# Kernel tuning notes

Hardware: AMD Instinct MI355X
Metric: run time of the kernel (lower is better)

Reference implementation:

```python
import jax, jax.numpy as jnp
import numpy as np

EPS = 1e-5
N_CONV = 3
B = 2048  # number of crystals


def _bn_eval(x, gamma, beta):
    # Eval-mode BatchNorm with running_mean=0, running_var=1.
    return x * (gamma / jnp.sqrt(1.0 + EPS)) + beta


def _conv_layer(atom_fea, nbr_fea, nbr_fea_idx, W, b, g1, b1, g2, b2):
    # Canonical CGCNN ConvLayer.
    N, M = nbr_fea_idx.shape
    F = atom_fea.shape[1]
    nbr_atom = atom_fea[nbr_fea_idx]                                  # [N,M,F]
    self_atom = jnp.broadcast_to(atom_fea[:, None, :], (N, M, F))     # [N,M,F]
    total = jnp.concatenate([self_atom, nbr_atom, nbr_fea], axis=2)   # [N,M,2F+nbr]
    gated = total @ W + b                                             # [N,M,2F]
    gated = _bn_eval(gated, g1, b1)
    flt, core = jnp.split(gated, 2, axis=2)
    nbr_sumed = jnp.sum(jax.nn.sigmoid(flt) * jax.nn.softplus(core), axis=1)  # [N,F]
    nbr_sumed = _bn_eval(nbr_sumed, g2, b2)
    return jax.nn.softplus(atom_fea + nbr_sumed)


def setup_inputs() -> dict:
    key = jax.random.key(0)
    ks = jax.random.split(key, 24)
    N, M = 60000, 12
    OA, NB, F, OE, E, H = 92, 41, 64, 8, 16, 128
    s = 0.05
    inp = {
        "atom_fea": jax.random.normal(ks[0], (N, OA), jnp.float32),
        "nbr_fea": jax.random.normal(ks[1], (N, M, NB), jnp.float32),
        "nbr_fea_idx": jax.random.randint(ks[2], (N, M), 0, N),
        "segment_ids": jnp.sort(jax.random.randint(ks[3], (N,), 0, B)),
        "extra_fea": jax.random.normal(ks[4], (B, OE), jnp.float32),
        # embedding_atom
        "W_embed": jax.random.normal(ks[5], (OA, F), jnp.float32) * s,
        "b_embed": jnp.zeros((F,), jnp.float32),
        # conv layers (stacked over n_conv=3)
        "conv_W": jax.random.normal(ks[6], (N_CONV, 2 * F + NB, 2 * F), jnp.float32) * s,
        "conv_b": jnp.zeros((N_CONV, 2 * F), jnp.float32),
        "bn1_g": jnp.ones((N_CONV, 2 * F), jnp.float32),
        "bn1_b": jnp.zeros((N_CONV, 2 * F), jnp.float32),
        "bn2_g": jnp.ones((N_CONV, F), jnp.float32),
        "bn2_b": jnp.zeros((N_CONV, F), jnp.float32),
        # embedding_extra
        "W_extra": jax.random.normal(ks[7], (OE, E), jnp.float32) * s,
        "b_extra": jnp.zeros((E,), jnp.float32),
        "bnx_g": jnp.ones((E,), jnp.float32),
        "bnx_b": jnp.zeros((E,), jnp.float32),
        # conv_to_fc
        "W_fc": jax.random.normal(ks[8], (F + E, H), jnp.float32) * s,
        "b_fc": jnp.zeros((H,), jnp.float32),
        "W_out0": jax.random.normal(ks[9], (H, 1), jnp.float32) * s,
        "b_out0": jnp.zeros((1,), jnp.float32),
        "W_out1": jax.random.normal(ks[10], (H, 2), jnp.float32) * s,
        "b_out1": jnp.zeros((2,), jnp.float32),
        "W_out2": jax.random.normal(ks[11], (H, 1), jnp.float32) * s,
        "b_out2": jnp.zeros((1,), jnp.float32),
    }
    return inp


def reference(atom_fea, nbr_fea, nbr_fea_idx, segment_ids, extra_fea,
              W_embed, b_embed, conv_W, conv_b, bn1_g, bn1_b, bn2_g, bn2_b,
              W_extra, b_extra, bnx_g, bnx_b, W_fc, b_fc,
              W_out0, b_out0, W_out1, b_out1, W_out2, b_out2):
    x = atom_fea @ W_embed + b_embed                                  # [N,F]
    extra = jax.nn.softplus(_bn_eval(extra_fea @ W_extra + b_extra, bnx_g, bnx_b))  # [B,E]
    for i in range(N_CONV):
        x = _conv_layer(x, nbr_fea, nbr_fea_idx, conv_W[i], conv_b[i],
                        bn1_g[i], bn1_b[i], bn2_g[i], bn2_b[i])
    # segment-mean pooling (replaces per-crystal python loop)
    sums = jax.ops.segment_sum(x, segment_ids, num_segments=B)        # [B,F]
    cnts = jax.ops.segment_sum(jnp.ones((x.shape[0],), x.dtype), segment_ids, num_segments=B)
    crys = sums / jnp.maximum(cnts, 1.0)[:, None]
    crys = jnp.concatenate([crys, extra], axis=1)                     # [B,F+E]
    crys = jax.nn.softplus(crys @ W_fc + b_fc)                        # [B,H]
    out0 = crys @ W_out0 + b_out0
    out1 = jax.nn.log_softmax(crys @ W_out1 + b_out1, axis=1)         # classification [B,2]
    out2 = crys @ W_out2 + b_out2
    return out0, out1, out2
```

## Files before the change

### kernel.cpp

```cpp
#include <hip/hip_runtime.h>
#include <math.h>
#include <stdint.h>

#define N_ATOMS 60000
#define M_NBR   12
#define NBF     41
#define B_CRYS  2048
#define EPSBN   1e-5f
#define GA      8
#define ROWS    (GA * M_NBR)
#define GRID_F  (N_ATOMS / GA)
#define WIMG_L  24576

typedef __attribute__((ext_vector_type(8))) short bf8;
typedef __attribute__((ext_vector_type(4))) float f32x4;
#define MFMA_B16(a, b, c) __builtin_amdgcn_mfma_f32_16x16x32_bf16(a, b, c, 0, 0, 0)

__device__ __forceinline__ short f2bf(float f) {
  uint32_t u = __builtin_bit_cast(uint32_t, f);
  u += 0x7FFFu + ((u >> 16) & 1u);
  return (short)(u >> 16);
}
__device__ __forceinline__ float lo16(uint32_t u) {
  return __builtin_bit_cast(float, u << 16);
}
__device__ __forceinline__ float hi16(uint32_t u) {
  return __builtin_bit_cast(float, u & 0xFFFF0000u);
}
__device__ __forceinline__ float sp(float x) {
  return (x > 15.f) ? x : __logf(1.f + __expf(x));
}
__device__ __forceinline__ float sig(float x) {
  return 1.f / (1.f + __expf(-x));
}

__global__ __launch_bounds__(256) void k_wprep(
    const float* __restrict__ conv_W, const float* __restrict__ conv_b,
    const float* __restrict__ bn1_g, const float* __restrict__ bn1_b,
    unsigned short* __restrict__ Wimg) {
  const int gid = blockIdx.x * 256 + threadIdx.x;
  if (gid >= 3 * WIMG_L) return;
  const int layer = gid / WIMG_L, rem = gid % WIMG_L;
  const int which = rem / 8192, r2 = rem % 8192;
  const int frag = r2 >> 9, lane = (r2 >> 3) & 63, j = r2 & 7;
  const int ct = frag >> 1, ks = frag & 1;
  const int quad = lane >> 4, l15 = lane & 15;
  const int jc = ct * 16 + l15;
  const int oc = (jc & 1) ? (jc >> 1) + 64 : (jc >> 1);
  const float s = bn1_g[layer * 128 + oc] * rsqrtf(1.f + EPSBN);
  const int k = ks * 32 + quad * 8 + j;
  const float* Wc = conv_W + (size_t)layer * 169 * 128;
  float v = 0.f;
  if (which == 0) {
    if (k < NBF) v = Wc[(128 + k) * 128 + oc] * s;
    else if (k == NBF) v = conv_b[layer * 128 + oc] * s + bn1_b[layer * 128 + oc];
  } else if (which == 1) {
    v = Wc[k * 128 + oc] * s;
  } else {
    v = Wc[(64 + k) * 128 + oc] * s;
  }
  Wimg[gid] = (unsigned short)f2bf(v);
}

__global__ __launch_bounds__(256) void k_embed2(
    const float* __restrict__ A, const float* __restrict__ W,
    const float* __restrict__ bias, float* __restrict__ X,
    unsigned int* __restrict__ XbU) {
  const int lane = threadIdx.x & 63, wv = threadIdx.x >> 6;
  const int quad = lane >> 4, l15 = lane & 15;
  const int gw = blockIdx.x * 4 + wv, nw = gridDim.x * 4;
  bf8 Bf[3][4];
  float bs[4];
#pragma unroll
  for (int ct = 0; ct < 4; ++ct) {
    const int col = ct * 16 + l15;
    bs[ct] = bias[col];
#pragma unroll
    for (int ks = 0; ks < 3; ++ks) {
      bf8 b;
#pragma unroll
      for (int i = 0; i < 8; ++i) {
        const int k = ks * 32 + quad * 8 + i;
        b[i] = (k < 92) ? f2bf(W[k * 64 + col]) : (short)0;
      }
      Bf[ks][ct] = b;
    }
  }
  for (int rt = gw; rt < 3750; rt += nw) {
    const int rbase = rt * 16;
    const float* ar = A + (size_t)(rbase + l15) * 92;
    const float4 p0 = *(const float4*)(ar + quad * 8);
    const float4 p1 = *(const float4*)(ar + quad * 8 + 4);
    const float4 p2 = *(const float4*)(ar + 32 + quad * 8);
    const float4 p3 = *(const float4*)(ar + 32 + quad * 8 + 4);
    bf8 A0, A1, A2;
    A0[0] = f2bf(p0.x); A0[1] = f2bf(p0.y); A0[2] = f2bf(p0.z); A0[3] = f2bf(p0.w);
    A0[4] = f2bf(p1.x); A0[5] = f2bf(p1.y); A0[6] = f2bf(p1.z); A0[7] = f2bf(p1.w);
    A1[0] = f2bf(p2.x); A1[1] = f2bf(p2.y); A1[2] = f2bf(p2.z); A1[3] = f2bf(p2.w);
    A1[4] = f2bf(p3.x); A1[5] = f2bf(p3.y); A1[6] = f2bf(p3.z); A1[7] = f2bf(p3.w);
#pragma unroll
    for (int i = 0; i < 8; ++i) {
      const int k = 64 + quad * 8 + i;
      A2[i] = (k < 92) ? f2bf(ar[k]) : (short)0;
    }
    const f32x4 z = {0.f, 0.f, 0.f, 0.f};
    f32x4 acc[4];
#pragma unroll
    for (int ct = 0; ct < 4; ++ct) {
      acc[ct] = MFMA_B16(A0, Bf[0][ct], z);
      acc[ct] = MFMA_B16(A1, Bf[1][ct], acc[ct]);
      acc[ct] = MFMA_B16(A2, Bf[2][ct], acc[ct]);
    }
#pragma unroll
    for (int ct = 0; ct < 4; ++ct)
#pragma unroll
      for (int r = 0; r < 4; ++r) {
        const int row = rbase + quad * 4 + r;
        const float v = acc[ct][r] + bs[ct];
        X[(size_t)row * 64 + ct * 16 + l15] = v;
        const unsigned int u = (unsigned short)f2bf(v);
        const unsigned int p = __shfl_xor((int)u, 1);
        if (!(l15 & 1))
          XbU[(size_t)row * 32 + ct * 8 + (l15 >> 1)] = u | (p << 16);
      }
  }
}

__global__ __launch_bounds__(256, 5) void k_fused4(
    float* __restrict__ X, const unsigned short* __restrict__ XbIn,
    unsigned int* __restrict__ XbOutU, const float* __restrict__ NF,
    const int* __restrict__ IDX, const unsigned short* __restrict__ Wi,
    const float* __restrict__ g2, const float* __restrict__ b2) {
  __shared__ __align__(16) unsigned int eb32[ROWS * 64];
  unsigned short* eb16 = (unsigned short*)eb32;
  float* stage = (float*)eb32;
  const int tid = threadIdx.x;
  const int lane = tid & 63, wv = tid >> 6;
  const int quad = lane >> 4, l15 = lane & 15;
  const int g = blockIdx.x;
  const int ntile = (wv < 2) ? 2 : 1;

  bf8 Ax0[2], Ax1[2], As0[2], As1[2];
#pragma unroll
  for (int ti = 0; ti < 2; ++ti) {
    if (ti < ntile) {
      const int rbase = (wv + ti * 4) * 16;
      const int jr = IDX[g * ROWS + rbase + l15];
      const unsigned short* xr = XbIn + (size_t)jr * 64 + quad * 8;
      Ax0[ti] = *(const bf8*)xr;
      Ax1[ti] = *(const bf8*)(xr + 32);
      const int arow = g * GA + (rbase + l15) / M_NBR;
      const unsigned short* sr = XbIn + (size_t)arow * 64 + quad * 8;
      As0[ti] = *(const bf8*)sr;
      As1[ti] = *(const bf8*)(sr + 32);
    }
  }

  const float4* s4 = (const float4*)(NF + (size_t)g * (ROWS * NBF));
#pragma unroll
  for (int it = 0; it < 4; ++it) {
    const int w = tid + it * 256;
    if (w < (ROWS * NBF) / 4) ((float4*)stage)[w] = s4[w];
  }
  __syncthreads();

  bf8 Ae0[2], Ae1[2];
#pragma unroll
  for (int ti = 0; ti < 2; ++ti) {
    if (ti < ntile) {
      const int rbase = (wv + ti * 4) * 16;
      const float* rp = stage + (rbase + l15) * NBF;
      bf8 a0, a1;
#pragma unroll
      for (int i = 0; i < 8; ++i) a0[i] = f2bf(rp[quad * 8 + i]);
      if (quad == 0) {
#pragma unroll
        for (int i = 0; i < 8; ++i) a1[i] = f2bf(rp[32 + i]);
      } else if (quad == 1) {
        a1[0] = f2bf(rp[40]);
        a1[1] = (short)0x3F80;
#pragma unroll
        for (int i = 2; i < 8; ++i) a1[i] = 0;
      } else {
#pragma unroll
        for (int i = 0; i < 8; ++i) a1[i] = 0;
      }
      Ae0[ti] = a0;
      Ae1[ti] = a1;
    }
  }
  __syncthreads();

#pragma unroll
  for (int ti = 0; ti < 2; ++ti) {
    if (ti < ntile) {
      const int rbase = (wv + ti * 4) * 16;
      const f32x4 z = {0.f, 0.f, 0.f, 0.f};
#pragma unroll 1
      for (int ct = 0; ct < 8; ++ct) {
        const bf8 Be0 = *(const bf8*)(Wi + ((ct * 2 + 0) * 64 + lane) * 8);
        const bf8 Be1 = *(const bf8*)(Wi + ((ct * 2 + 1) * 64 + lane) * 8);
        const bf8 Bs0 =
            *(const bf8*)(Wi + 8192 + ((ct * 2 + 0) * 64 + lane) * 8);
        const bf8 Bs1 =
            *(const bf8*)(Wi + 8192 + ((ct * 2 + 1) * 64 + lane) * 8);
        const bf8 Bn0 =
            *(const bf8*)(Wi + 16384 + ((ct * 2 + 0) * 64 + lane) * 8);
        const bf8 Bn1 =
            *(const bf8*)(Wi + 16384 + ((ct * 2 + 1) * 64 + lane) * 8);
        f32x4 acc = MFMA_B16(Ax0[ti], Bn0, z);
        acc = MFMA_B16(Ax1[ti], Bn1, acc);
        acc = MFMA_B16(As0[ti], Bs0, acc);
        acc = MFMA_B16(As1[ti], Bs1, acc);
        acc = MFMA_B16(Ae0[ti], Be0, acc);
        acc = MFMA_B16(Ae1[ti], Be1, acc);
        const int j = ct * 16 + l15;
        const int c = j >> 1, h = j & 1;
#pragma unroll
        for (int r = 0; r < 4; ++r) {
          const int row = rbase + quad * 4 + r;
          eb16[row * 128 + ((c + row) & 63) * 2 + h] =
              (unsigned short)f2bf(acc[r]);
        }
      }
    }
  }
  __syncthreads();

  const float inv = rsqrtf(1.f + EPSBN);
  const float s2 = g2[lane] * inv, o2 = b2[lane];
#pragma unroll
  for (int al = 0; al < 2; ++al) {
    const int a_local = wv * 2 + al;
    const int n = g * GA + a_local;
    float acc = 0.f;
#pragma unroll
    for (int m = 0; m < 12; ++m) {
      const int row = a_local * 12 + m;
      const uint32_t eu = eb32[row * 64 + ((lane + row) & 63)];
      acc += sig(lo16(eu)) * sp(hi16(eu));
    }
    const size_t o = (size_t)n * 64 + lane;
    const float res = sp(X[o] + acc * s2 + o2);
    X[o] = res;
    const unsigned int u = (unsigned short)f2bf(res);
    const unsigned int p = __shfl_xor((int)u, 1);
    if (!(lane & 1)) XbOutU[(size_t)n * 32 + (lane >> 1)] = u | (p << 16);
  }
}

__device__ __forceinline__ int lbound(const int* __restrict__ a, int n, int v) {
  int lo = 0, hi = n;
  while (lo < hi) {
    int mid = (lo + hi) >> 1;
    if (a[mid] < v) lo = mid + 1; else hi = mid;
  }
  return lo;
}

__global__ __launch_bounds__(128) void k_head(
    const float* __restrict__ Xf, const int* __restrict__ seg,
    const float* __restrict__ EF, const float* __restrict__ Wx,
    const float* __restrict__ bx, const float* __restrict__ gx,
    const float* __restrict__ bxb, const float* __restrict__ Wfc,
    const float* __restrict__ bfc, const float* __restrict__ Wo0,
    const float* __restrict__ bo0, const float* __restrict__ Wo1,
    const float* __restrict__ bo1, const float* __restrict__ Wo2,
    const float* __restrict__ bo2, float* __restrict__ out) {
  const int b = blockIdx.x;
  const int t = threadIdx.x;
  __shared__ float vbuf[80];
  __shared__ float part[128];
  __shared__ float4 r4[128];
  const int lo = lbound(seg, N_ATOMS, b);
  const int hi = lbound(seg, N_ATOMS, b + 1);
  const int col = t & 63, half = t >> 6;
  float s = 0.f;
  for (int r = lo + half; r < hi; r += 2) s += Xf[(size_t)r * 64 + col];
  part[t] = s;
  __syncthreads();
  if (t < 64) {
    vbuf[t] = (part[t] + part[t + 64]) / fmaxf((float)(hi - lo), 1.f);
  } else if (t < 80) {
    const int e = t - 64;
    float a = bx[e];
#pragma unroll
    for (int k = 0; k < 8; ++k) a += EF[b * 8 + k] * Wx[k * 16 + e];
    a = a * (gx[e] * rsqrtf(1.f + EPSBN)) + bxb[e];
    vbuf[t] = sp(a);
  }
  __syncthreads();
  float h = bfc[t];
#pragma unroll
  for (int k = 0; k < 80; ++k) h += vbuf[k] * Wfc[k * 128 + t];
  h = sp(h);
  r4[t] = make_float4(h * Wo0[t], h * Wo1[2 * t], h * Wo1[2 * t + 1],
                      h * Wo2[t]);
  __syncthreads();
  for (int st2 = 64; st2 > 0; st2 >>= 1) {
    if (t < st2) {
      float4 a = r4[t], c = r4[t + st2];
      r4[t] = make_float4(a.x + c.x, a.y + c.y, a.z + c.z, a.w + c.w);
    }
    __syncthreads();
  }
  if (t == 0) {
    float4 r = r4[0];
    out[b] = r.x + bo0[0];
    float z0 = r.y + bo1[0], z1 = r.z + bo1[1];
    float mx = fmaxf(z0, z1);
    float lse = mx + __logf(__expf(z0 - mx) + __expf(z1 - mx));
    out[B_CRYS + 2 * b] = z0 - lse;
    out[B_CRYS + 2 * b + 1] = z1 - lse;
    out[3 * B_CRYS + b] = r.w + bo2[0];
  }
}

extern "C" void kernel_launch(void* const* d_in, const int* in_sizes, int n_in,
                              void* d_out, int out_size, void* d_ws,
                              size_t ws_size, hipStream_t stream) {
  const float* atom_fea = (const float*)d_in[0];
  const float* nbr_fea  = (const float*)d_in[1];
  const int*   nbr_idx  = (const int*)d_in[2];
  const int*   seg      = (const int*)d_in[3];
  const float* extra    = (const float*)d_in[4];
  const float* W_embed  = (const float*)d_in[5];
  const float* b_embed  = (const float*)d_in[6];
  const float* conv_W   = (const float*)d_in[7];
  const float* conv_b   = (const float*)d_in[8];
  const float* bn1_g    = (const float*)d_in[9];
  const float* bn1_b    = (const float*)d_in[10];
  const float* bn2_g    = (const float*)d_in[11];
  const float* bn2_b    = (const float*)d_in[12];
  const float* W_extra  = (const float*)d_in[13];
  const float* b_extra  = (const float*)d_in[14];
  const float* bnx_g    = (const float*)d_in[15];
  const float* bnx_b    = (const float*)d_in[16];
  const float* W_fc     = (const float*)d_in[17];
  const float* b_fc     = (const float*)d_in[18];
  const float* W_out0   = (const float*)d_in[19];
  const float* b_out0   = (const float*)d_in[20];
  const float* W_out1   = (const float*)d_in[21];
  const float* b_out1   = (const float*)d_in[22];
  const float* W_out2   = (const float*)d_in[23];
  const float* b_out2   = (const float*)d_in[24];
  float* out = (float*)d_out;

  float* x = (float*)d_ws;
  unsigned int* xbu0 = (unsigned int*)(x + (size_t)N_ATOMS * 64);
  unsigned int* xbu1 = xbu0 + (size_t)N_ATOMS * 32;
  unsigned short* Wimg = (unsigned short*)(xbu1 + (size_t)N_ATOMS * 32);

  hipLaunchKernelGGL(k_wprep, dim3((3 * WIMG_L) / 256), dim3(256), 0, stream,
                     conv_W, conv_b, bn1_g, bn1_b, Wimg);
  hipLaunchKernelGGL(k_embed2, dim3(960), dim3(256), 0, stream, atom_fea,
                     W_embed, b_embed, x, xbu0);
  unsigned int* xin = xbu0;
  unsigned int* xout = xbu1;
  for (int i = 0; i < 3; ++i) {
    hipLaunchKernelGGL(k_fused4, dim3(GRID_F), dim3(256), 0, stream, x,
                       (const unsigned short*)xin, xout, nbr_fea, nbr_idx,
                       Wimg + (size_t)i * WIMG_L, bn2_g + i * 64,
                       bn2_b + i * 64);
    unsigned int* tmp = xin;
    xin = xout;
    xout = tmp;
  }
  hipLaunchKernelGGL(k_head, dim3(B_CRYS), dim3(128), 0, stream, x, seg, extra,
                     W_extra, b_extra, bnx_g, bnx_b, W_fc, b_fc, W_out0, b_out0,
                     W_out1, b_out1, W_out2, b_out2, out);
}
```

Measured before the change: 565.2 us.

## Reduce gated outputs in registers with shuffles instead of an LDS round trip

The conv kernel now gives each wave one atom per 16-row MFMA tile: 12 neighbor rows are used and 4 are padding. The sigmoid·softplus gating and the neighbor sum are done directly on the accumulators through cross-lane shuffles, so the bf16 LDS staging buffer and its extra barrier pass are gone. Neighbor features are converted to bf16 once into a smaller padded LDS buffer, and the occupancy hint rises from 5 to 6. In exchange, a quarter of the MFMA rows do wasted work, since the tile count per block goes from 6 to 8, and the per-tile loop adds shuffle and transcendental overhead.

```diff
diff --git a/kernel.cpp b/kernel.cpp
--- a/kernel.cpp
+++ b/kernel.cpp
@@ -8,9 +8,9 @@
 #define B_CRYS  2048
 #define EPSBN   1e-5f
 #define GA      8
-#define ROWS    (GA * M_NBR)
 #define GRID_F  (N_ATOMS / GA)
 #define WIMG_L  24576
+#define SSTR    56
 
 typedef __attribute__((ext_vector_type(8))) short bf8;
 typedef __attribute__((ext_vector_type(4))) float f32x4;
@@ -20,12 +20,6 @@
   uint32_t u = __builtin_bit_cast(uint32_t, f);
   u += 0x7FFFu + ((u >> 16) & 1u);
   return (short)(u >> 16);
-}
-__device__ __forceinline__ float lo16(uint32_t u) {
-  return __builtin_bit_cast(float, u << 16);
-}
-__device__ __forceinline__ float hi16(uint32_t u) {
-  return __builtin_bit_cast(float, u & 0xFFFF0000u);
 }
 __device__ __forceinline__ float sp(float x) {
   return (x > 15.f) ? x : __logf(1.f + __expf(x));
@@ -126,126 +120,85 @@
   }
 }
 
-__global__ __launch_bounds__(256, 5) void k_fused4(
+__global__ __launch_bounds__(256, 6) void k_fused5(
     float* __restrict__ X, const unsigned short* __restrict__ XbIn,
     unsigned int* __restrict__ XbOutU, const float* __restrict__ NF,
     const int* __restrict__ IDX, const unsigned short* __restrict__ Wi,
     const float* __restrict__ g2, const float* __restrict__ b2) {
-  __shared__ __align__(16) unsigned int eb32[ROWS * 64];
-  unsigned short* eb16 = (unsigned short*)eb32;
-  float* stage = (float*)eb32;
+  __shared__ __align__(16) unsigned short sfea[96 * SSTR];
   const int tid = threadIdx.x;
   const int lane = tid & 63, wv = tid >> 6;
   const int quad = lane >> 4, l15 = lane & 15;
   const int g = blockIdx.x;
-  const int ntile = (wv < 2) ? 2 : 1;
-
-  bf8 Ax0[2], Ax1[2], As0[2], As1[2];
-#pragma unroll
+  const float inv = rsqrtf(1.f + EPSBN);
+
+  const float* src = NF + (size_t)g * (96 * NBF);
+  for (int e = tid; e < 96 * NBF; e += 256) {
+    const int row = e / NBF, col = e - row * NBF;
+    sfea[row * SSTR + col] = (unsigned short)f2bf(src[e]);
+  }
+  __syncthreads();
+
+#pragma unroll 1
   for (int ti = 0; ti < 2; ++ti) {
-    if (ti < ntile) {
-      const int rbase = (wv + ti * 4) * 16;
-      const int jr = IDX[g * ROWS + rbase + l15];
-      const unsigned short* xr = XbIn + (size_t)jr * 64 + quad * 8;
-      Ax0[ti] = *(const bf8*)xr;
-      Ax1[ti] = *(const bf8*)(xr + 32);
-      const int arow = g * GA + (rbase + l15) / M_NBR;
-      const unsigned short* sr = XbIn + (size_t)arow * 64 + quad * 8;
-      As0[ti] = *(const bf8*)sr;
-      As1[ti] = *(const bf8*)(sr + 32);
-    }
-  }
-
-  const float4* s4 = (const float4*)(NF + (size_t)g * (ROWS * NBF));
-#pragma unroll
-  for (int it = 0; it < 4; ++it) {
-    const int w = tid + it * 256;
-    if (w < (ROWS * NBF) / 4) ((float4*)stage)[w] = s4[w];
-  }
-  __syncthreads();
-
-  bf8 Ae0[2], Ae1[2];
-#pragma unroll
-  for (int ti = 0; ti < 2; ++ti) {
-    if (ti < ntile) {
-      const int rbase = (wv + ti * 4) * 16;
-      const float* rp = stage + (rbase + l15) * NBF;
-      bf8 a0, a1;
-#pragma unroll
-      for (int i = 0; i < 8; ++i) a0[i] = f2bf(rp[quad * 8 + i]);
-      if (quad == 0) {
-#pragma unroll
-        for (int i = 0; i < 8; ++i) a1[i] = f2bf(rp[32 + i]);
-      } else if (quad == 1) {
-        a1[0] = f2bf(rp[40]);
-        a1[1] = (short)0x3F80;
-#pragma unroll
-        for (int i = 2; i < 8; ++i) a1[i] = 0;
-      } else {
-#pragma unroll
-        for (int i = 0; i < 8; ++i) a1[i] = 0;
+    const int rt = wv * 2 + ti;
+    const int n = g * GA + rt;
+    const int li = (l15 < 12) ? l15 : 11;
+    const int jr = IDX[n * 12 + li];
+    const unsigned short* xr = XbIn + (size_t)jr * 64 + quad * 8;
+    const bf8 Ax0 = *(const bf8*)xr;
+    const bf8 Ax1 = *(const bf8*)(xr + 32);
+    const unsigned short* sr = XbIn + (size_t)n * 64 + quad * 8;
+    const bf8 As0 = *(const bf8*)sr;
+    const bf8 As1 = *(const bf8*)(sr + 32);
+    const unsigned short* ep = sfea + (rt * 12 + li) * SSTR;
+    const bf8 Ae0 = *(const bf8*)(ep + quad * 8);
+    bf8 Ae1 = {0, 0, 0, 0, 0, 0, 0, 0};
+    if (quad < 2) Ae1 = *(const bf8*)(ep + 32 + quad * 8);
+    if (quad == 1) {
+      Ae1[1] = (short)0x3F80;
+#pragma unroll
+      for (int i = 2; i < 8; ++i) Ae1[i] = 0;
+    }
+
+    const f32x4 z = {0.f, 0.f, 0.f, 0.f};
+#pragma unroll 1
+    for (int ct = 0; ct < 8; ++ct) {
+      const bf8 Be0 = *(const bf8*)(Wi + ((ct * 2 + 0) * 64 + lane) * 8);
+      const bf8 Be1 = *(const bf8*)(Wi + ((ct * 2 + 1) * 64 + lane) * 8);
+      const bf8 Bs0 = *(const bf8*)(Wi + 8192 + ((ct * 2 + 0) * 64 + lane) * 8);
+      const bf8 Bs1 = *(const bf8*)(Wi + 8192 + ((ct * 2 + 1) * 64 + lane) * 8);
+      const bf8 Bn0 = *(const bf8*)(Wi + 16384 + ((ct * 2 + 0) * 64 + lane) * 8);
+      const bf8 Bn1 = *(const bf8*)(Wi + 16384 + ((ct * 2 + 1) * 64 + lane) * 8);
+      f32x4 acc = MFMA_B16(Ax0, Bn0, z);
+      acc = MFMA_B16(Ax1, Bn1, acc);
+      acc = MFMA_B16(As0, Bs0, acc);
+      acc = MFMA_B16(As1, Bs1, acc);
+      acc = MFMA_B16(Ae0, Be0, acc);
+      acc = MFMA_B16(Ae1, Be1, acc);
+      float t0 = __shfl_xor(acc[0], 1);
+      float t1 = __shfl_xor(acc[1], 1);
+      float t2 = __shfl_xor(acc[2], 1);
+      float t3 = __shfl_xor(acc[3], 1);
+      const bool odd = (l15 & 1);
+      const float f0 = odd ? t2 : acc[0];
+      const float c0 = odd ? acc[2] : t0;
+      const float f1 = odd ? t3 : acc[1];
+      const float c1 = odd ? acc[3] : t1;
+      float p = sig(f0) * sp(c0) + sig(f1) * sp(c1);
+      if (quad == 3) p = 0.f;
+      p += __shfl_xor(p, 1);
+      p += __shfl_xor(p, 16);
+      p += __shfl_xor(p, 32);
+      if ((ct >> 1) == quad) {
+        const int c = ct * 8 + (l15 >> 1);
+        const float res = sp(X[(size_t)n * 64 + c] + p * (g2[c] * inv) + b2[c]);
+        const unsigned int u = (unsigned short)f2bf(res);
+        const unsigned int pu = __shfl_xor((int)u, 2);
+        if (!(l15 & 1)) X[(size_t)n * 64 + c] = res;
+        if (!(l15 & 3)) XbOutU[(size_t)n * 32 + (c >> 1)] = u | (pu << 16);
       }
-      Ae0[ti] = a0;
-      Ae1[ti] = a1;
-    }
-  }
-  __syncthreads();
-
-#pragma unroll
-  for (int ti = 0; ti < 2; ++ti) {
-    if (ti < ntile) {
-      const int rbase = (wv + ti * 4) * 16;
-      const f32x4 z = {0.f, 0.f, 0.f, 0.f};
-#pragma unroll 1
-      for (int ct = 0; ct < 8; ++ct) {
-        const bf8 Be0 = *(const bf8*)(Wi + ((ct * 2 + 0) * 64 + lane) * 8);
-        const bf8 Be1 = *(const bf8*)(Wi + ((ct * 2 + 1) * 64 + lane) * 8);
-        const bf8 Bs0 =
-            *(const bf8*)(Wi + 8192 + ((ct * 2 + 0) * 64 + lane) * 8);
-        const bf8 Bs1 =
-            *(const bf8*)(Wi + 8192 + ((ct * 2 + 1) * 64 + lane) * 8);
-        const bf8 Bn0 =
-            *(const bf8*)(Wi + 16384 + ((ct * 2 + 0) * 64 + lane) * 8);
-        const bf8 Bn1 =
-            *(const bf8*)(Wi + 16384 + ((ct * 2 + 1) * 64 + lane) * 8);
-        f32x4 acc = MFMA_B16(Ax0[ti], Bn0, z);
-        acc = MFMA_B16(Ax1[ti], Bn1, acc);
-        acc = MFMA_B16(As0[ti], Bs0, acc);
-        acc = MFMA_B16(As1[ti], Bs1, acc);
-        acc = MFMA_B16(Ae0[ti], Be0, acc);
-        acc = MFMA_B16(Ae1[ti], Be1, acc);
-        const int j = ct * 16 + l15;
-        const int c = j >> 1, h = j & 1;
-#pragma unroll
-        for (int r = 0; r < 4; ++r) {
-          const int row = rbase + quad * 4 + r;
-          eb16[row * 128 + ((c + row) & 63) * 2 + h] =
-              (unsigned short)f2bf(acc[r]);
-        }
-      }
-    }
-  }
-  __syncthreads();
-
-  const float inv = rsqrtf(1.f + EPSBN);
-  const float s2 = g2[lane] * inv, o2 = b2[lane];
-#pragma unroll
-  for (int al = 0; al < 2; ++al) {
-    const int a_local = wv * 2 + al;
-    const int n = g * GA + a_local;
-    float acc = 0.f;
-#pragma unroll
-    for (int m = 0; m < 12; ++m) {
-      const int row = a_local * 12 + m;
-      const uint32_t eu = eb32[row * 64 + ((lane + row) & 63)];
-      acc += sig(lo16(eu)) * sp(hi16(eu));
-    }
-    const size_t o = (size_t)n * 64 + lane;
-    const float res = sp(X[o] + acc * s2 + o2);
-    X[o] = res;
-    const unsigned int u = (unsigned short)f2bf(res);
-    const unsigned int p = __shfl_xor((int)u, 1);
-    if (!(lane & 1)) XbOutU[(size_t)n * 32 + (lane >> 1)] = u | (p << 16);
+    }
   }
 }
 
@@ -358,7 +311,7 @@
   unsigned int* xin = xbu0;
   unsigned int* xout = xbu1;
   for (int i = 0; i < 3; ++i) {
-    hipLaunchKernelGGL(k_fused4, dim3(GRID_F), dim3(256), 0, stream, x,
+    hipLaunchKernelGGL(k_fused5, dim3(GRID_F), dim3(256), 0, stream, x,
                        (const unsigned short*)xin, xout, nbr_fea, nbr_idx,
                        Wimg + (size_t)i * WIMG_L, bn2_g + i * 64,
                        bn2_b + i * 64);
```

After: 732.8 us. +29.7%, slower.
